# Optimization experiments

Hardware: AMD Instinct MI355X
Metric: run time of the kernel (lower is better)

The kernel has to match this reference:

```python
import jax, jax.numpy as jnp
import numpy as np

N = 20000   # nodes
E = 320000  # edges (avg degree 16)
K = 3       # Chebyshev order


def _glorot(key, shape):
    fan_in, fan_out = shape[-2], shape[-1]
    lim = (6.0 / (fan_in + fan_out)) ** 0.5
    return jax.random.uniform(key, shape, minval=-lim, maxval=lim, dtype=jnp.float32)


def setup_inputs() -> dict:
    key = jax.random.key(0)
    ks = jax.random.split(key, 8)
    v = jax.random.normal(ks[0], (N, 86), dtype=jnp.float32)
    edges = jax.random.randint(ks[1], (2, E), 0, N, dtype=jnp.int32)
    W1 = _glorot(ks[2], (K, 86, 128));  b1 = jnp.zeros((128,), jnp.float32)
    W2 = _glorot(ks[3], (K, 128, 256)); b2 = jnp.zeros((256,), jnp.float32)
    W3 = _glorot(ks[4], (K, 256, 512)); b3 = jnp.zeros((512,), jnp.float32)
    return {"v": v, "edges": edges, "W1": W1, "b1": b1,
            "W2": W2, "b2": b2, "W3": W3, "b3": b3}


def _cheb_norm(edges, n):
    # PyG ChebConv with sym norm, lambda_max=2: L_hat = L - I = -D^-1/2 A D^-1/2
    # (diagonal entries from get_laplacian (+1) and add_self_loops (-1) cancel).
    # Self loops are removed before computing the Laplacian -> mask them out.
    row, col = edges[0], edges[1]
    w = (row != col).astype(jnp.float32)
    deg = jax.ops.segment_sum(w, row, num_segments=n)
    dinv = jnp.where(deg > 0, jax.lax.rsqrt(jnp.maximum(deg, 1e-12)), 0.0)
    norm_w = -dinv[row] * w * dinv[col]  # [E]
    return row, col, norm_w


def _cheb_conv(x, row, col, norm_w, W, b):
    # W: [K, in, out]
    def prop(z):  # L_hat @ z via edge gather + segment scatter-add
        return jax.ops.segment_sum(norm_w[:, None] * z[col], row, num_segments=x.shape[0])
    Tx0 = x
    out = Tx0 @ W[0]
    Tx1 = prop(Tx0)
    out = out + Tx1 @ W[1]
    Tx2 = 2.0 * prop(Tx1) - Tx0
    out = out + Tx2 @ W[2]
    return out + b


def reference(v, edges, W1, b1, W2, b2, W3, b3):
    row, col, norm_w = _cheb_norm(edges, v.shape[0])
    nk = jax.random.key(42)
    x1 = jax.nn.relu(_cheb_conv(v, row, col, norm_w, W1, b1))
    x1 = x1 * jax.random.normal(jax.random.fold_in(nk, 1), x1.shape, x1.dtype)
    x2 = jax.nn.relu(_cheb_conv(x1, row, col, norm_w, W2, b2))
    x2 = x2 * jax.random.normal(jax.random.fold_in(nk, 2), x2.shape, x2.dtype)
    x3 = jax.nn.relu(_cheb_conv(x2, row, col, norm_w, W3, b3))
    x3 = x3 * jax.random.normal(jax.random.fold_in(nk, 3), x3.shape, x3.dtype)
    return (x1, x2, x3)
```

## Files before the change

kernel.cpp:

```cpp
#include <hip/hip_runtime.h>
#include <stdint.h>
#include <math.h>

#define DEV static __device__ __forceinline__

typedef __attribute__((ext_vector_type(8))) short bf16x8;
typedef __attribute__((ext_vector_type(4))) float f32x4;
typedef __attribute__((ext_vector_type(8))) unsigned short u16x8;

DEV uint32_t rotl32(uint32_t v, int d) { return (v << d) | (v >> (32 - d)); }

DEV void threefry2x32(uint32_t k0, uint32_t k1, uint32_t& x0, uint32_t& x1) {
  const uint32_t k2 = k0 ^ k1 ^ 0x1BD11BDAu;
  x0 += k0; x1 += k1;
#define TFR(R) { x0 += x1; x1 = rotl32(x1, R) ^ x0; }
  TFR(13) TFR(15) TFR(26) TFR(6)
  x0 += k1; x1 += k2 + 1u;
  TFR(17) TFR(29) TFR(16) TFR(24)
  x0 += k2; x1 += k0 + 2u;
  TFR(13) TFR(15) TFR(26) TFR(6)
  x0 += k0; x1 += k1 + 3u;
  TFR(17) TFR(29) TFR(16) TFR(24)
  x0 += k1; x1 += k2 + 4u;
  TFR(13) TFR(15) TFR(26) TFR(6)
  x0 += k2; x1 += k0 + 5u;
#undef TFR
}

DEV float erfinv_f32(float x) {
  float w = -log1pf(-x * x);
  float p;
  if (w < 5.0f) {
    w -= 2.5f;
    p = 2.81022636e-08f;
    p = fmaf(p, w, 3.43273939e-07f);
    p = fmaf(p, w, -3.5233877e-06f);
    p = fmaf(p, w, -4.39150654e-06f);
    p = fmaf(p, w, 0.00021858087f);
    p = fmaf(p, w, -0.00125372503f);
    p = fmaf(p, w, -0.00417768164f);
    p = fmaf(p, w, 0.246640727f);
    p = fmaf(p, w, 1.50140941f);
  } else {
    w = sqrtf(w) - 3.0f;
    p = -0.000200214257f;
    p = fmaf(p, w, 0.000100950558f);
    p = fmaf(p, w, 0.00134934322f);
    p = fmaf(p, w, -0.00367342844f);
    p = fmaf(p, w, 0.00573950773f);
    p = fmaf(p, w, -0.0076224613f);
    p = fmaf(p, w, 0.00943887047f);
    p = fmaf(p, w, 1.00167406f);
    p = fmaf(p, w, 2.83297682f);
  }
  return p * x;
}

DEV float normal_from_bits(uint32_t bits) {
  float f = __uint_as_float((bits >> 9) | 0x3F800000u) - 1.0f;
  const float lo = -0.99999994f;
  float u = fmaf(f, 2.0f, lo);
  u = fmaxf(u, lo);
  return 1.41421356f * erfinv_f32(u);
}

DEV unsigned short f2bf(float f) {
  uint32_t u = __float_as_uint(f);
  uint32_t r = u + 0x7FFFu + ((u >> 16) & 1u);
  return (unsigned short)(r >> 16);
}

DEV float bf2f(uint32_t h) { return __uint_as_float(h << 16); }

DEV float4 noise4(uint32_t f0, uint32_t f1, uint32_t i4) {
  uint32_t base = i4 * 4u;
  float4 r;
  { uint32_t a = 0u, b = base + 0u; threefry2x32(f0, f1, a, b); r.x = normal_from_bits(a ^ b); }
  { uint32_t a = 0u, b = base + 1u; threefry2x32(f0, f1, a, b); r.y = normal_from_bits(a ^ b); }
  { uint32_t a = 0u, b = base + 2u; threefry2x32(f0, f1, a, b); r.z = normal_from_bits(a ^ b); }
  { uint32_t a = 0u, b = base + 3u; threefry2x32(f0, f1, a, b); r.w = normal_from_bits(a ^ b); }
  return r;
}

__global__ void count_kernel(const int* __restrict__ rows, const int* __restrict__ cols,
                             int* __restrict__ counts, int* __restrict__ degs, int E) {
  int e = blockIdx.x * blockDim.x + threadIdx.x;
  if (e < E) {
    int r = rows[e];
    atomicAdd(&counts[r], 1);
    if (r != cols[e]) atomicAdd(&degs[r], 1);
  }
}

#define SCAN_T 1024
__global__ __launch_bounds__(SCAN_T) void scan_kernel(const int* __restrict__ counts,
                                                      int* __restrict__ row_ptr,
                                                      int* __restrict__ cursor, int N) {
  __shared__ int sa[SCAN_T], sb[SCAN_T];
  const int t = threadIdx.x;
  const int CH = (N + SCAN_T - 1) / SCAN_T;
  int base = t * CH;
  int psum = 0;
  for (int k = 0; k < CH; ++k) {
    int idx = base + k;
    if (idx < N) psum += counts[idx];
  }
  sa[t] = psum;
  __syncthreads();
  int* src = sa; int* dst = sb;
  for (int off = 1; off < SCAN_T; off <<= 1) {
    int v = src[t];
    if (t >= off) v += src[t - off];
    dst[t] = v;
    __syncthreads();
    int* tmp = src; src = dst; dst = tmp;
  }
  int running = src[t] - psum;
  for (int k = 0; k < CH; ++k) {
    int idx = base + k;
    if (idx < N) {
      row_ptr[idx] = running;
      cursor[idx] = running;
      running += counts[idx];
    }
  }
  if (t == SCAN_T - 1) row_ptr[N] = running;
}

__global__ void fill_kernel(const int* __restrict__ rows, const int* __restrict__ cols,
                            const int* __restrict__ degs, int* __restrict__ cursor,
                            float2* __restrict__ ecv, int E) {
  int e = blockIdx.x * blockDim.x + threadIdx.x;
  if (e < E) {
    int r = rows[e], c = cols[e];
    int dr = degs[r], dc = degs[c];
    float w = (r != c && dr > 0 && dc > 0) ? -rsqrtf((float)dr) * rsqrtf((float)dc) : 0.0f;
    int pos = atomicAdd(&cursor[r], 1);
    ecv[pos] = make_float2(__int_as_float(c), w);
  }
}

template <int VEC>
DEV void ldrow(const unsigned short* base, size_t off, float* v) {
  const unsigned short* p = base + off;
  if (VEC == 4) {
    uint2 u = *(const uint2*)p;
    v[0] = bf2f(u.x & 0xffffu); v[1] = bf2f(u.x >> 16);
    v[2] = bf2f(u.y & 0xffffu); v[3] = bf2f(u.y >> 16);
  } else {
    uint32_t u = *(const uint32_t*)p;
    v[0] = bf2f(u & 0xffffu); v[1] = bf2f(u >> 16);
  }
}

template <int VEC, int SUB, int FOLD>
__global__ __launch_bounds__(256) void gather_prop(
    const int* __restrict__ row_ptr, const float2* __restrict__ ecv,
    const unsigned short* __restrict__ xsrc, int sstride,
    const float* __restrict__ xsub, int substride,
    unsigned short* __restrict__ outb, int N, int F, int Fpad,
    float* __restrict__ nbuf, int n4_begin, int n4_end) {
  const int wave = threadIdx.x >> 6, lane = threadIdx.x & 63;
  const int node = blockIdx.x * 4 + wave;
  const int f0 = lane * VEC;
  if (node < N && f0 < Fpad) {
    const bool live = (f0 + VEC) <= F;
    float acc[VEC] = {};
    if (live) {
      const int s = row_ptr[node], e = row_ptr[node + 1];
      int j = s;
      for (; j + 8 <= e; j += 8) {
        float2 cw[8];
        float vv[8][VEC];
#pragma unroll
        for (int q = 0; q < 8; ++q) cw[q] = ecv[j + q];
#pragma unroll
        for (int q = 0; q < 8; ++q)
          ldrow<VEC>(xsrc, (size_t)__float_as_int(cw[q].x) * sstride + f0, vv[q]);
#pragma unroll
        for (int q = 0; q < 8; ++q)
#pragma unroll
          for (int z = 0; z < VEC; ++z) acc[z] = fmaf(cw[q].y, vv[q][z], acc[z]);
      }
      for (; j + 2 <= e; j += 2) {
        float2 cw[2];
        float vv[2][VEC];
#pragma unroll
        for (int q = 0; q < 2; ++q) cw[q] = ecv[j + q];
#pragma unroll
        for (int q = 0; q < 2; ++q)
          ldrow<VEC>(xsrc, (size_t)__float_as_int(cw[q].x) * sstride + f0, vv[q]);
#pragma unroll
        for (int q = 0; q < 2; ++q)
#pragma unroll
          for (int z = 0; z < VEC; ++z) acc[z] = fmaf(cw[q].y, vv[q][z], acc[z]);
      }
      for (; j < e; ++j) {
        float2 cw = ecv[j];
        float vv[VEC];
        ldrow<VEC>(xsrc, (size_t)__float_as_int(cw.x) * sstride + f0, vv);
#pragma unroll
        for (int z = 0; z < VEC; ++z) acc[z] = fmaf(cw.y, vv[z], acc[z]);
      }
      if (SUB) {
        const float* sb = xsub + (size_t)node * substride + f0;
#pragma unroll
        for (int z = 0; z < VEC; ++z) acc[z] = fmaf(2.0f, acc[z], -sb[z]);
      }
    }
    size_t ob = (size_t)node * Fpad + f0;
    if (VEC == 4) {
      uint2 u;
      u.x = (uint32_t)f2bf(acc[0]) | ((uint32_t)f2bf(acc[1]) << 16);
      u.y = (uint32_t)f2bf(acc[2]) | ((uint32_t)f2bf(acc[3]) << 16);
      *(uint2*)&outb[ob] = u;
    } else {
      uint32_t u = (uint32_t)f2bf(acc[0]) | ((uint32_t)f2bf(acc[1]) << 16);
      *(uint32_t*)&outb[ob] = u;
    }
  }
  uint32_t f0k = 0u, f1k = (uint32_t)FOLD;
  threefry2x32(0u, 42u, f0k, f1k);
  const int gstride = gridDim.x * 256;
  for (int i4 = n4_begin + blockIdx.x * 256 + threadIdx.x; i4 < n4_end; i4 += gstride) {
    float4 r = noise4(f0k, f1k, (uint32_t)i4);
    *(float4*)&nbuf[(size_t)i4 * 4] = r;
  }
}

__global__ void wtrans_kernel(const float* __restrict__ W, unsigned short* __restrict__ Wt,
                              int F, int Fpad, int O) {
  int idx = blockIdx.x * 256 + threadIdx.x;
  int total = 3 * O * Fpad;
  if (idx >= total) return;
  int k = idx % Fpad;
  int o = (idx / Fpad) % O;
  int p = idx / (Fpad * O);
  Wt[idx] = (k < F) ? f2bf(W[((size_t)p * F + k) * O + o]) : (unsigned short)0;
}

__global__ void vconv_kernel(const float* __restrict__ v, unsigned short* __restrict__ vb, int N) {
  int i = blockIdx.x * 256 + threadIdx.x;
  if (i >= N * 96) return;
  int r = i / 96, k = i % 96;
  vb[i] = (k < 86) ? f2bf(v[(size_t)r * 86 + k]) : (unsigned short)0;
}

template <int BM, int FPAD, int KS>
__global__ __launch_bounds__(512, 4) void gemm3_db(
    const unsigned short* __restrict__ A0, const unsigned short* __restrict__ A1,
    const unsigned short* __restrict__ A2,
    const unsigned short* __restrict__ Wt, const float* __restrict__ bias,
    const float* __restrict__ noise,
    int M, int O, float* __restrict__ out, unsigned short* __restrict__ outb,
    int obstride) {
  constexpr int BN = 128;
  constexpr int NSP = FPAD / KS;
  constexpr int NSTEP = 3 * NSP;
  constexpr int CPR = KS / 8;
  constexpr int LST = KS + 8;
  constexpr int NA = BM * CPR;
  constexpr int NB = BN * CPR;
  constexpr int ACH = (NA + 511) / 512;
  constexpr int BCH = (NB + 511) / 512;
  constexpr int MFR = BM / 32;
  constexpr int KK = KS / 32;

  __shared__ unsigned short sA[2][BM * LST];
  __shared__ unsigned short sB[2][BN * LST];

  const int tid = threadIdx.x;
  const int lane = tid & 63;
  const int wave = tid >> 6;
  const int wm = wave >> 2, wo = wave & 3;
  const int bm = blockIdx.x * BM;
  const int bo = blockIdx.y * BN;
  const int l15 = lane & 15;
  const int kg = (lane >> 4) * 8;

  f32x4 acc[MFR][2] = {};
  const unsigned short* As[3] = {A0, A1, A2};

  u16x8 ra0[ACH], rb0[BCH], ra1[ACH], rb1[BCH];

  auto issue = [&](int s, u16x8 (&ra)[ACH], u16x8 (&rb)[BCH]) {
    int p = s / NSP, k0 = (s % NSP) * KS;
    const unsigned short* __restrict__ A = As[p];
    const unsigned short* __restrict__ B = Wt + (size_t)p * O * FPAD;
#pragma unroll
    for (int c = 0; c < ACH; ++c) {
      int idx = tid + c * 512;
      if (NA % 512 == 0 || idx < NA) {
        int row = idx / CPR, ch = (idx % CPR) * 8;
        int gm = bm + row; if (gm >= M) gm = M - 1;
        ra[c] = *(const u16x8*)(A + (size_t)gm * FPAD + k0 + ch);
      }
    }
#pragma unroll
    for (int c = 0; c < BCH; ++c) {
      int idx = tid + c * 512;
      if (NB % 512 == 0 || idx < NB) {
        int row = idx / CPR, ch = (idx % CPR) * 8;
        rb[c] = *(const u16x8*)(B + (size_t)(bo + row) * FPAD + k0 + ch);
      }
    }
  };

  auto lds_write = [&](int buf, u16x8 (&ra)[ACH], u16x8 (&rb)[BCH]) {
#pragma unroll
    for (int c = 0; c < ACH; ++c) {
      int idx = tid + c * 512;
      if (NA % 512 == 0 || idx < NA) {
        int row = idx / CPR, ch = (idx % CPR) * 8;
        *(u16x8*)&sA[buf][row * LST + ch] = ra[c];
      }
    }
#pragma unroll
    for (int c = 0; c < BCH; ++c) {
      int idx = tid + c * 512;
      if (NB % 512 == 0 || idx < NB) {
        int row = idx / CPR, ch = (idx % CPR) * 8;
        *(u16x8*)&sB[buf][row * LST + ch] = rb[c];
      }
    }
  };

  auto compute = [&](int buf) {
#pragma unroll
    for (int kk = 0; kk < KK; ++kk) {
      bf16x8 af[MFR], bfr[2];
#pragma unroll
      for (int mi = 0; mi < MFR; ++mi)
        af[mi] = *(const bf16x8*)&sA[buf][(wm * (BM / 2) + mi * 16 + l15) * LST + kk * 32 + kg];
#pragma unroll
      for (int ni = 0; ni < 2; ++ni)
        bfr[ni] = *(const bf16x8*)&sB[buf][(wo * 32 + ni * 16 + l15) * LST + kk * 32 + kg];
#pragma unroll
      for (int mi = 0; mi < MFR; ++mi)
#pragma unroll
        for (int ni = 0; ni < 2; ++ni)
          acc[mi][ni] = __builtin_amdgcn_mfma_f32_16x16x32_bf16(af[mi], bfr[ni], acc[mi][ni], 0, 0, 0);
    }
  };

  issue(0, ra0, rb0);
  issue(1, ra1, rb1);
  lds_write(0, ra0, rb0);
  __syncthreads();

#pragma unroll
  for (int s = 0; s < NSTEP; ++s) {
    if ((s & 1) == 0) {
      if (s + 2 < NSTEP) issue(s + 2, ra0, rb0);
      compute(s & 1);
      if (s + 1 < NSTEP) { lds_write((s + 1) & 1, ra1, rb1); __syncthreads(); }
    } else {
      if (s + 2 < NSTEP) issue(s + 2, ra1, rb1);
      compute(s & 1);
      if (s + 1 < NSTEP) { lds_write((s + 1) & 1, ra0, rb0); __syncthreads(); }
    }
  }

  const int r0 = (lane >> 4) * 4;
#pragma unroll
  for (int mi = 0; mi < MFR; ++mi) {
#pragma unroll
    for (int r = 0; r < 4; ++r) {
      int gm = bm + wm * (BM / 2) + mi * 16 + r0 + r;
      if (gm >= M) continue;
#pragma unroll
      for (int ni = 0; ni < 2; ++ni) {
        int go = bo + wo * 32 + ni * 16 + l15;
        float vv = acc[mi][ni][r] + bias[go];
        vv = vv > 0.0f ? vv : 0.0f;
        float res = vv * noise[(size_t)gm * O + go];
        out[(size_t)gm * O + go] = res;
        if (outb) outb[(size_t)gm * obstride + go] = f2bf(res);
      }
    }
  }
}

extern "C" void kernel_launch(void* const* d_in, const int* in_sizes, int n_in,
                              void* d_out, int out_size, void* d_ws, size_t ws_size,
                              hipStream_t stream) {
  const float* v    = (const float*)d_in[0];
  const int*  edges = (const int*)d_in[1];
  const float* W1 = (const float*)d_in[2];
  const float* b1 = (const float*)d_in[3];
  const float* W2 = (const float*)d_in[4];
  const float* b2 = (const float*)d_in[5];
  const float* W3 = (const float*)d_in[6];
  const float* b3 = (const float*)d_in[7];
  float* out = (float*)d_out;

  const int N = in_sizes[0] / 86;
  const int E = in_sizes[1] / 2;
  const int* rows = edges;
  const int* cols = edges + E;

  uintptr_t cur = (uintptr_t)d_ws;
  auto alloc = [&](size_t bytes) {
    cur = (cur + 15) & ~(uintptr_t)15;
    void* p = (void*)cur;
    cur += bytes;
    return p;
  };
  float2* ecv          = (float2*)alloc((size_t)E * 8);
  int* counts          = (int*)alloc((size_t)N * 4);
  int* degs            = (int*)alloc((size_t)N * 4);
  int* row_ptr         = (int*)alloc((size_t)(N + 1) * 4);
  int* cursor          = (int*)alloc((size_t)N * 4);
  unsigned short* tx1b = (unsigned short*)alloc((size_t)N * 256 * 2);
  unsigned short* tx2b = (unsigned short*)alloc((size_t)N * 256 * 2);
  unsigned short* vb   = (unsigned short*)alloc((size_t)N * 96 * 2);
  unsigned short* x1b  = (unsigned short*)alloc((size_t)N * 128 * 2);
  unsigned short* x2b  = (unsigned short*)alloc((size_t)N * 256 * 2);
  unsigned short* Wt   = (unsigned short*)alloc((size_t)3 * 512 * 256 * 2);
  float* nbuf          = (float*)alloc((size_t)N * 512 * 4);

  float* x1 = out;
  float* x2 = x1 + (size_t)N * 128;
  float* x3 = x2 + (size_t)N * 256;

  hipMemsetAsync(counts, 0, (size_t)2 * N * sizeof(int), stream);
  count_kernel<<<(E + 255) / 256, 256, 0, stream>>>(rows, cols, counts, degs, E);
  scan_kernel<<<1, SCAN_T, 0, stream>>>(counts, row_ptr, cursor, N);
  fill_kernel<<<(E + 255) / 256, 256, 0, stream>>>(rows, cols, degs, cursor, ecv, E);
  vconv_kernel<<<(N * 96 + 255) / 256, 256, 0, stream>>>(v, vb, N);

  const int pblocks = (N + 3) / 4;

  {
    wtrans_kernel<<<(3 * 128 * 96 + 255) / 256, 256, 0, stream>>>(W1, Wt, 86, 96, 128);
    int t4 = N * 128 / 4, h4 = t4 / 2;
    gather_prop<2, 0, 1><<<pblocks, 256, 0, stream>>>(row_ptr, ecv, vb, 96, nullptr, 0, tx1b, N, 86, 96, nbuf, 0, h4);
    gather_prop<2, 1, 1><<<pblocks, 256, 0, stream>>>(row_ptr, ecv, tx1b, 96, v, 86, tx2b, N, 86, 96, nbuf, h4, t4);
    dim3 g((N + 63) / 64, 1);
    gemm3_db<64, 96, 32><<<g, 512, 0, stream>>>(vb, tx1b, tx2b, Wt, b1, nbuf, N, 128, x1, x1b, 128);
  }
  {
    wtrans_kernel<<<(3 * 256 * 128 + 255) / 256, 256, 0, stream>>>(W2, Wt, 128, 128, 256);
    int t4 = N * 256 / 4, h4 = t4 / 2;
    gather_prop<2, 0, 2><<<pblocks, 256, 0, stream>>>(row_ptr, ecv, x1b, 128, nullptr, 0, tx1b, N, 128, 128, nbuf, 0, h4);
    gather_prop<2, 1, 2><<<pblocks, 256, 0, stream>>>(row_ptr, ecv, tx1b, 128, x1, 128, tx2b, N, 128, 128, nbuf, h4, t4);
    dim3 g((N + 127) / 128, 2);
    gemm3_db<128, 128, 64><<<g, 512, 0, stream>>>(x1b, tx1b, tx2b, Wt, b2, nbuf, N, 256, x2, x2b, 256);
  }
  {
    wtrans_kernel<<<(3 * 512 * 256 + 255) / 256, 256, 0, stream>>>(W3, Wt, 256, 256, 512);
    int t4 = N * 512 / 4, h4 = t4 / 2;
    gather_prop<4, 0, 3><<<pblocks, 256, 0, stream>>>(row_ptr, ecv, x2b, 256, nullptr, 0, tx1b, N, 256, 256, nbuf, 0, h4);
    gather_prop<4, 1, 3><<<pblocks, 256, 0, stream>>>(row_ptr, ecv, tx1b, 256, x2, 256, tx2b, N, 256, 256, nbuf, h4, t4);
    dim3 g((N + 127) / 128, 4);
    gemm3_db<128, 256, 64><<<g, 512, 0, stream>>>(x2b, tx1b, tx2b, Wt, b3, nbuf, N, 512, x3, nullptr, 0);
  }
}
```

Measured before the change: 370.3 us.

## Pack multiple nodes per wave with 16-byte gathers, bf16 noise, fused prep, XCD tile remap

The neighbor gather now assigns several nodes per wavefront, each lane loading 8 bf16 features at once, so lanes no longer sit idle on narrow feature widths. The dropout noise buffer is stored as bf16 instead of fp32, halving its write and read traffic. The input conversion and all three weight transposes are fused into one prep kernel launched once. GEMM blocks are remapped so consecutive M tiles land on the same XCD for L2 reuse. Storing noise in bf16 adds rounding error to the output multiplier.

```diff
diff --git a/kernel.cpp b/kernel.cpp
--- a/kernel.cpp
+++ b/kernel.cpp
@@ -140,119 +140,138 @@
   }
 }
 
-template <int VEC>
-DEV void ldrow(const unsigned short* base, size_t off, float* v) {
-  const unsigned short* p = base + off;
-  if (VEC == 4) {
-    uint2 u = *(const uint2*)p;
-    v[0] = bf2f(u.x & 0xffffu); v[1] = bf2f(u.x >> 16);
-    v[2] = bf2f(u.y & 0xffffu); v[3] = bf2f(u.y >> 16);
-  } else {
-    uint32_t u = *(const uint32_t*)p;
-    v[0] = bf2f(u & 0xffffu); v[1] = bf2f(u >> 16);
-  }
-}
-
-template <int VEC, int SUB, int FOLD>
+__global__ void prep_kernel(const float* __restrict__ v,
+                            const float* __restrict__ W1, const float* __restrict__ W2,
+                            const float* __restrict__ W3,
+                            unsigned short* __restrict__ vb, unsigned short* __restrict__ wt1,
+                            unsigned short* __restrict__ wt2, unsigned short* __restrict__ wt3,
+                            int N) {
+  int i = blockIdx.x * 256 + threadIdx.x;
+  int nv = N * 96;
+  if (i < nv) {
+    int r = i / 96, k = i % 96;
+    vb[i] = (k < 86) ? f2bf(v[(size_t)r * 86 + k]) : (unsigned short)0;
+    return;
+  }
+  i -= nv;
+  if (i < 3 * 128 * 96) {
+    int k = i % 96, o = (i / 96) % 128, p = i / (96 * 128);
+    wt1[i] = (k < 86) ? f2bf(W1[((size_t)p * 86 + k) * 128 + o]) : (unsigned short)0;
+    return;
+  }
+  i -= 3 * 128 * 96;
+  if (i < 3 * 256 * 128) {
+    int k = i % 128, o = (i / 128) % 256, p = i / (128 * 256);
+    wt2[i] = f2bf(W2[((size_t)p * 128 + k) * 256 + o]);
+    return;
+  }
+  i -= 3 * 256 * 128;
+  if (i < 3 * 512 * 256) {
+    int k = i % 256, o = (i / 256) % 512, p = i / (256 * 512);
+    wt3[i] = f2bf(W3[((size_t)p * 256 + k) * 512 + o]);
+  }
+}
+
+DEV void ld8(const unsigned short* __restrict__ base, size_t off, float* v) {
+  uint4 u = *(const uint4*)(base + off);
+  v[0] = bf2f(u.x & 0xffffu); v[1] = bf2f(u.x >> 16);
+  v[2] = bf2f(u.y & 0xffffu); v[3] = bf2f(u.y >> 16);
+  v[4] = bf2f(u.z & 0xffffu); v[5] = bf2f(u.z >> 16);
+  v[6] = bf2f(u.w & 0xffffu); v[7] = bf2f(u.w >> 16);
+}
+
+template <int LPN, int NL, int SUB, int FOLD>
 __global__ __launch_bounds__(256) void gather_prop(
     const int* __restrict__ row_ptr, const float2* __restrict__ ecv,
     const unsigned short* __restrict__ xsrc, int sstride,
-    const float* __restrict__ xsub, int substride,
-    unsigned short* __restrict__ outb, int N, int F, int Fpad,
-    float* __restrict__ nbuf, int n4_begin, int n4_end) {
+    const float* __restrict__ xsub, int substride, int F,
+    unsigned short* __restrict__ outb, int N, int Fpad,
+    unsigned short* __restrict__ nbuf, int n4_begin, int n4_end) {
   const int wave = threadIdx.x >> 6, lane = threadIdx.x & 63;
-  const int node = blockIdx.x * 4 + wave;
-  const int f0 = lane * VEC;
-  if (node < N && f0 < Fpad) {
-    const bool live = (f0 + VEC) <= F;
-    float acc[VEC] = {};
-    if (live) {
-      const int s = row_ptr[node], e = row_ptr[node + 1];
-      int j = s;
-      for (; j + 8 <= e; j += 8) {
-        float2 cw[8];
-        float vv[8][VEC];
-#pragma unroll
-        for (int q = 0; q < 8; ++q) cw[q] = ecv[j + q];
-#pragma unroll
-        for (int q = 0; q < 8; ++q)
-          ldrow<VEC>(xsrc, (size_t)__float_as_int(cw[q].x) * sstride + f0, vv[q]);
-#pragma unroll
-        for (int q = 0; q < 8; ++q)
-#pragma unroll
-          for (int z = 0; z < VEC; ++z) acc[z] = fmaf(cw[q].y, vv[q][z], acc[z]);
-      }
-      for (; j + 2 <= e; j += 2) {
-        float2 cw[2];
-        float vv[2][VEC];
-#pragma unroll
-        for (int q = 0; q < 2; ++q) cw[q] = ecv[j + q];
-#pragma unroll
-        for (int q = 0; q < 2; ++q)
-          ldrow<VEC>(xsrc, (size_t)__float_as_int(cw[q].x) * sstride + f0, vv[q]);
-#pragma unroll
-        for (int q = 0; q < 2; ++q)
-#pragma unroll
-          for (int z = 0; z < VEC; ++z) acc[z] = fmaf(cw[q].y, vv[q][z], acc[z]);
-      }
-      for (; j < e; ++j) {
-        float2 cw = ecv[j];
-        float vv[VEC];
-        ldrow<VEC>(xsrc, (size_t)__float_as_int(cw.x) * sstride + f0, vv);
-#pragma unroll
-        for (int z = 0; z < VEC; ++z) acc[z] = fmaf(cw.y, vv[z], acc[z]);
-      }
-      if (SUB) {
-        const float* sb = xsub + (size_t)node * substride + f0;
-#pragma unroll
-        for (int z = 0; z < VEC; ++z) acc[z] = fmaf(2.0f, acc[z], -sb[z]);
-      }
-    }
-    size_t ob = (size_t)node * Fpad + f0;
-    if (VEC == 4) {
-      uint2 u;
-      u.x = (uint32_t)f2bf(acc[0]) | ((uint32_t)f2bf(acc[1]) << 16);
-      u.y = (uint32_t)f2bf(acc[2]) | ((uint32_t)f2bf(acc[3]) << 16);
-      *(uint2*)&outb[ob] = u;
-    } else {
-      uint32_t u = (uint32_t)f2bf(acc[0]) | ((uint32_t)f2bf(acc[1]) << 16);
-      *(uint32_t*)&outb[ob] = u;
-    }
+  const int sub = lane / LPN;
+  const int fl = (lane - sub * LPN) * 8;
+  const int node = (blockIdx.x * 4 + wave) * NL + sub;
+  if (sub < NL && node < N) {
+    float acc[8] = {};
+    const int s = row_ptr[node], e = row_ptr[node + 1];
+    int j = s;
+    for (; j + 8 <= e; j += 8) {
+      float2 cw[8];
+      float vv[8][8];
+#pragma unroll
+      for (int q = 0; q < 8; ++q) cw[q] = ecv[j + q];
+#pragma unroll
+      for (int q = 0; q < 8; ++q)
+        ld8(xsrc, (size_t)__float_as_int(cw[q].x) * sstride + fl, vv[q]);
+#pragma unroll
+      for (int q = 0; q < 8; ++q)
+#pragma unroll
+        for (int z = 0; z < 8; ++z) acc[z] = fmaf(cw[q].y, vv[q][z], acc[z]);
+    }
+    for (; j + 2 <= e; j += 2) {
+      float2 cw[2];
+      float vv[2][8];
+#pragma unroll
+      for (int q = 0; q < 2; ++q) cw[q] = ecv[j + q];
+#pragma unroll
+      for (int q = 0; q < 2; ++q)
+        ld8(xsrc, (size_t)__float_as_int(cw[q].x) * sstride + fl, vv[q]);
+#pragma unroll
+      for (int q = 0; q < 2; ++q)
+#pragma unroll
+        for (int z = 0; z < 8; ++z) acc[z] = fmaf(cw[q].y, vv[q][z], acc[z]);
+    }
+    for (; j < e; ++j) {
+      float2 cw = ecv[j];
+      float vv[8];
+      ld8(xsrc, (size_t)__float_as_int(cw.x) * sstride + fl, vv);
+#pragma unroll
+      for (int z = 0; z < 8; ++z) acc[z] = fmaf(cw.y, vv[z], acc[z]);
+    }
+    if (SUB) {
+      const float* sb = xsub + (size_t)node * substride;
+      if (fl + 8 <= F) {
+        float4 a = *(const float4*)(sb + fl);
+        float4 b2 = *(const float4*)(sb + fl + 4);
+        acc[0] = fmaf(2.0f, acc[0], -a.x);  acc[1] = fmaf(2.0f, acc[1], -a.y);
+        acc[2] = fmaf(2.0f, acc[2], -a.z);  acc[3] = fmaf(2.0f, acc[3], -a.w);
+        acc[4] = fmaf(2.0f, acc[4], -b2.x); acc[5] = fmaf(2.0f, acc[5], -b2.y);
+        acc[6] = fmaf(2.0f, acc[6], -b2.z); acc[7] = fmaf(2.0f, acc[7], -b2.w);
+      } else {
+#pragma unroll
+        for (int z = 0; z < 8; ++z) {
+          int f = fl + z;
+          float sv = (f < F) ? sb[f] : 0.0f;
+          acc[z] = fmaf(2.0f, acc[z], -sv);
+        }
+      }
+    }
+    uint4 u;
+    u.x = (uint32_t)f2bf(acc[0]) | ((uint32_t)f2bf(acc[1]) << 16);
+    u.y = (uint32_t)f2bf(acc[2]) | ((uint32_t)f2bf(acc[3]) << 16);
+    u.z = (uint32_t)f2bf(acc[4]) | ((uint32_t)f2bf(acc[5]) << 16);
+    u.w = (uint32_t)f2bf(acc[6]) | ((uint32_t)f2bf(acc[7]) << 16);
+    *(uint4*)&outb[(size_t)node * Fpad + fl] = u;
   }
   uint32_t f0k = 0u, f1k = (uint32_t)FOLD;
   threefry2x32(0u, 42u, f0k, f1k);
   const int gstride = gridDim.x * 256;
-  for (int i4 = n4_begin + blockIdx.x * 256 + threadIdx.x; i4 < n4_end; i4 += gstride) {
+  for (int i4 = n4_begin + blockIdx.x * 256 + (int)threadIdx.x; i4 < n4_end; i4 += gstride) {
     float4 r = noise4(f0k, f1k, (uint32_t)i4);
-    *(float4*)&nbuf[(size_t)i4 * 4] = r;
-  }
-}
-
-__global__ void wtrans_kernel(const float* __restrict__ W, unsigned short* __restrict__ Wt,
-                              int F, int Fpad, int O) {
-  int idx = blockIdx.x * 256 + threadIdx.x;
-  int total = 3 * O * Fpad;
-  if (idx >= total) return;
-  int k = idx % Fpad;
-  int o = (idx / Fpad) % O;
-  int p = idx / (Fpad * O);
-  Wt[idx] = (k < F) ? f2bf(W[((size_t)p * F + k) * O + o]) : (unsigned short)0;
-}
-
-__global__ void vconv_kernel(const float* __restrict__ v, unsigned short* __restrict__ vb, int N) {
-  int i = blockIdx.x * 256 + threadIdx.x;
-  if (i >= N * 96) return;
-  int r = i / 96, k = i % 96;
-  vb[i] = (k < 86) ? f2bf(v[(size_t)r * 86 + k]) : (unsigned short)0;
-}
-
-template <int BM, int FPAD, int KS>
+    uint2 u;
+    u.x = (uint32_t)f2bf(r.x) | ((uint32_t)f2bf(r.y) << 16);
+    u.y = (uint32_t)f2bf(r.z) | ((uint32_t)f2bf(r.w) << 16);
+    *(uint2*)&nbuf[(size_t)i4 * 4] = u;
+  }
+}
+
+template <int BM, int FPAD, int KS, int OB>
 __global__ __launch_bounds__(512, 4) void gemm3_db(
     const unsigned short* __restrict__ A0, const unsigned short* __restrict__ A1,
     const unsigned short* __restrict__ A2,
     const unsigned short* __restrict__ Wt, const float* __restrict__ bias,
-    const float* __restrict__ noise,
-    int M, int O, float* __restrict__ out, unsigned short* __restrict__ outb,
+    const unsigned short* __restrict__ noise,
+    int M, int MT, int O, float* __restrict__ out, unsigned short* __restrict__ outb,
     int obstride) {
   constexpr int BN = 128;
   constexpr int NSP = FPAD / KS;
@@ -266,6 +285,14 @@
   constexpr int MFR = BM / 32;
   constexpr int KK = KS / 32;
 
+  const int flat = blockIdx.x;
+  const int xcd = flat & 7, idx = flat >> 3;
+  const int mtile = xcd + 8 * (idx / OB);
+  const int obl = idx - (idx / OB) * OB;
+  if (mtile >= MT) return;
+  const int bm = mtile * BM;
+  const int bo = obl * BN;
+
   __shared__ unsigned short sA[2][BM * LST];
   __shared__ unsigned short sB[2][BN * LST];
 
@@ -273,8 +300,6 @@
   const int lane = tid & 63;
   const int wave = tid >> 6;
   const int wm = wave >> 2, wo = wave & 3;
-  const int bm = blockIdx.x * BM;
-  const int bo = blockIdx.y * BN;
   const int l15 = lane & 15;
   const int kg = (lane >> 4) * 8;
 
@@ -289,18 +314,18 @@
     const unsigned short* __restrict__ B = Wt + (size_t)p * O * FPAD;
 #pragma unroll
     for (int c = 0; c < ACH; ++c) {
-      int idx = tid + c * 512;
-      if (NA % 512 == 0 || idx < NA) {
-        int row = idx / CPR, ch = (idx % CPR) * 8;
+      int idx2 = tid + c * 512;
+      if (NA % 512 == 0 || idx2 < NA) {
+        int row = idx2 / CPR, ch = (idx2 % CPR) * 8;
         int gm = bm + row; if (gm >= M) gm = M - 1;
         ra[c] = *(const u16x8*)(A + (size_t)gm * FPAD + k0 + ch);
       }
     }
 #pragma unroll
     for (int c = 0; c < BCH; ++c) {
-      int idx = tid + c * 512;
-      if (NB % 512 == 0 || idx < NB) {
-        int row = idx / CPR, ch = (idx % CPR) * 8;
+      int idx2 = tid + c * 512;
+      if (NB % 512 == 0 || idx2 < NB) {
+        int row = idx2 / CPR, ch = (idx2 % CPR) * 8;
         rb[c] = *(const u16x8*)(B + (size_t)(bo + row) * FPAD + k0 + ch);
       }
     }
@@ -309,17 +334,17 @@
   auto lds_write = [&](int buf, u16x8 (&ra)[ACH], u16x8 (&rb)[BCH]) {
 #pragma unroll
     for (int c = 0; c < ACH; ++c) {
-      int idx = tid + c * 512;
-      if (NA % 512 == 0 || idx < NA) {
-        int row = idx / CPR, ch = (idx % CPR) * 8;
+      int idx2 = tid + c * 512;
+      if (NA % 512 == 0 || idx2 < NA) {
+        int row = idx2 / CPR, ch = (idx2 % CPR) * 8;
         *(u16x8*)&sA[buf][row * LST + ch] = ra[c];
       }
     }
 #pragma unroll
     for (int c = 0; c < BCH; ++c) {
-      int idx = tid + c * 512;
-      if (NB % 512 == 0 || idx < NB) {
-        int row = idx / CPR, ch = (idx % CPR) * 8;
+      int idx2 = tid + c * 512;
+      if (NB % 512 == 0 || idx2 < NB) {
+        int row = idx2 / CPR, ch = (idx2 % CPR) * 8;
         *(u16x8*)&sB[buf][row * LST + ch] = rb[c];
       }
     }
@@ -373,7 +398,7 @@
         int go = bo + wo * 32 + ni * 16 + l15;
         float vv = acc[mi][ni][r] + bias[go];
         vv = vv > 0.0f ? vv : 0.0f;
-        float res = vv * noise[(size_t)gm * O + go];
+        float res = vv * bf2f((uint32_t)noise[(size_t)gm * O + go]);
         out[(size_t)gm * O + go] = res;
         if (outb) outb[(size_t)gm * obstride + go] = f2bf(res);
       }
@@ -416,8 +441,10 @@
   unsigned short* vb   = (unsigned short*)alloc((size_t)N * 96 * 2);
   unsigned short* x1b  = (unsigned short*)alloc((size_t)N * 128 * 2);
   unsigned short* x2b  = (unsigned short*)alloc((size_t)N * 256 * 2);
-  unsigned short* Wt   = (unsigned short*)alloc((size_t)3 * 512 * 256 * 2);
-  float* nbuf          = (float*)alloc((size_t)N * 512 * 4);
+  unsigned short* wt1  = (unsigned short*)alloc((size_t)3 * 128 * 96 * 2);
+  unsigned short* wt2  = (unsigned short*)alloc((size_t)3 * 256 * 128 * 2);
+  unsigned short* wt3  = (unsigned short*)alloc((size_t)3 * 512 * 256 * 2);
+  unsigned short* nbuf = (unsigned short*)alloc((size_t)N * 512 * 2);
 
   float* x1 = out;
   float* x2 = x1 + (size_t)N * 128;
@@ -427,32 +454,36 @@
   count_kernel<<<(E + 255) / 256, 256, 0, stream>>>(rows, cols, counts, degs, E);
   scan_kernel<<<1, SCAN_T, 0, stream>>>(counts, row_ptr, cursor, N);
   fill_kernel<<<(E + 255) / 256, 256, 0, stream>>>(rows, cols, degs, cursor, ecv, E);
-  vconv_kernel<<<(N * 96 + 255) / 256, 256, 0, stream>>>(v, vb, N);
-
-  const int pblocks = (N + 3) / 4;
-
   {
-    wtrans_kernel<<<(3 * 128 * 96 + 255) / 256, 256, 0, stream>>>(W1, Wt, 86, 96, 128);
+    int total = N * 96 + 3 * 128 * 96 + 3 * 256 * 128 + 3 * 512 * 256;
+    prep_kernel<<<(total + 255) / 256, 256, 0, stream>>>(v, W1, W2, W3, vb, wt1, wt2, wt3, N);
+  }
+
+  {
+    int pb = (N + 15) / 16;
     int t4 = N * 128 / 4, h4 = t4 / 2;
-    gather_prop<2, 0, 1><<<pblocks, 256, 0, stream>>>(row_ptr, ecv, vb, 96, nullptr, 0, tx1b, N, 86, 96, nbuf, 0, h4);
-    gather_prop<2, 1, 1><<<pblocks, 256, 0, stream>>>(row_ptr, ecv, tx1b, 96, v, 86, tx2b, N, 86, 96, nbuf, h4, t4);
-    dim3 g((N + 63) / 64, 1);
-    gemm3_db<64, 96, 32><<<g, 512, 0, stream>>>(vb, tx1b, tx2b, Wt, b1, nbuf, N, 128, x1, x1b, 128);
+    gather_prop<12, 4, 0, 1><<<pb, 256, 0, stream>>>(row_ptr, ecv, vb, 96, nullptr, 0, 86, tx1b, N, 96, nbuf, 0, h4);
+    gather_prop<12, 4, 1, 1><<<pb, 256, 0, stream>>>(row_ptr, ecv, tx1b, 96, v, 86, 86, tx2b, N, 96, nbuf, h4, t4);
+    int mt = (N + 63) / 64;
+    int grid = 8 * ((mt + 7) / 8) * 1;
+    gemm3_db<64, 96, 32, 1><<<grid, 512, 0, stream>>>(vb, tx1b, tx2b, wt1, b1, nbuf, N, mt, 128, x1, x1b, 128);
   }
   {
-    wtrans_kernel<<<(3 * 256 * 128 + 255) / 256, 256, 0, stream>>>(W2, Wt, 128, 128, 256);
+    int pb = (N + 15) / 16;
     int t4 = N * 256 / 4, h4 = t4 / 2;
-    gather_prop<2, 0, 2><<<pblocks, 256, 0, stream>>>(row_ptr, ecv, x1b, 128, nullptr, 0, tx1b, N, 128, 128, nbuf, 0, h4);
-    gather_prop<2, 1, 2><<<pblocks, 256, 0, stream>>>(row_ptr, ecv, tx1b, 128, x1, 128, tx2b, N, 128, 128, nbuf, h4, t4);
-    dim3 g((N + 127) / 128, 2);
-    gemm3_db<128, 128, 64><<<g, 512, 0, stream>>>(x1b, tx1b, tx2b, Wt, b2, nbuf, N, 256, x2, x2b, 256);
+    gather_prop<16, 4, 0, 2><<<pb, 256, 0, stream>>>(row_ptr, ecv, x1b, 128, nullptr, 0, 128, tx1b, N, 128, nbuf, 0, h4);
+    gather_prop<16, 4, 1, 2><<<pb, 256, 0, stream>>>(row_ptr, ecv, tx1b, 128, x1, 128, 128, tx2b, N, 128, nbuf, h4, t4);
+    int mt = (N + 127) / 128;
+    int grid = 8 * ((mt + 7) / 8) * 2;
+    gemm3_db<128, 128, 64, 2><<<grid, 512, 0, stream>>>(x1b, tx1b, tx2b, wt2, b2, nbuf, N, mt, 256, x2, x2b, 256);
   }
   {
-    wtrans_kernel<<<(3 * 512 * 256 + 255) / 256, 256, 0, stream>>>(W3, Wt, 256, 256, 512);
+    int pb = (N + 7) / 8;
     int t4 = N * 512 / 4, h4 = t4 / 2;
-    gather_prop<4, 0, 3><<<pblocks, 256, 0, stream>>>(row_ptr, ecv, x2b, 256, nullptr, 0, tx1b, N, 256, 256, nbuf, 0, h4);
-    gather_prop<4, 1, 3><<<pblocks, 256, 0, stream>>>(row_ptr, ecv, tx1b, 256, x2, 256, tx2b, N, 256, 256, nbuf, h4, t4);
-    dim3 g((N + 127) / 128, 4);
-    gemm3_db<128, 256, 64><<<g, 512, 0, stream>>>(x2b, tx1b, tx2b, Wt, b3, nbuf, N, 512, x3, nullptr, 0);
-  }
-}
+    gather_prop<32, 2, 0, 3><<<pb, 256, 0, stream>>>(row_ptr, ecv, x2b, 256, nullptr, 0, 256, tx1b, N, 256, nbuf, 0, h4);
+    gather_prop<32, 2, 1, 3><<<pb, 256, 0, stream>>>(row_ptr, ecv, tx1b, 256, x2, 256, 256, tx2b, N, 256, nbuf, h4, t4);
+    int mt = (N + 127) / 128;
+    int grid = 8 * ((mt + 7) / 8) * 4;
+    gemm3_db<128, 256, 64, 4><<<grid, 512, 0, stream>>>(x2b, tx1b, tx2b, wt3, b3, nbuf, N, mt, 512, x3, nullptr, 0);
+  }
+}
```

Result: faster. 360.7 us (-2.6%).
